# Kernel optimization log

Hardware: AMD Instinct MI355X
Metric: run time of the kernel (lower is better)

The kernel has to match this reference:

```python
import jax, jax.numpy as jnp
import numpy as np

N_RAYS, N_SAMPLES, N_VERTS = 2048, 32, 6890

def setup_inputs() -> dict:
    key = jax.random.key(0)
    k1, k2, k3, k4 = jax.random.split(key, 4)
    rays_points_world = jax.random.normal(k1, (1, N_RAYS, 1, N_SAMPLES, 3), jnp.float32)
    rays_directions_world = jax.random.normal(k2, (1, N_RAYS, 1, N_SAMPLES, 3), jnp.float32)
    vertices_posed = jax.random.normal(k3, (1, N_VERTS, 3), jnp.float32)
    # Ts must be invertible: small perturbation of identity (like rigid bone transforms)
    Ts = jax.random.normal(k4, (1, N_VERTS, 4, 4), jnp.float32) * 0.1 + jnp.eye(4, dtype=jnp.float32)
    return {
        'rays_points_world': rays_points_world,
        'rays_directions_world': rays_directions_world,
        'vertices_posed': vertices_posed,
        'Ts': Ts,
    }

def reference(rays_points_world, rays_directions_world, vertices_posed, Ts):
    orig_shape = rays_points_world.shape  # [1, R, 1, S, 3]
    pts = rays_points_world.reshape(-1, 3)          # (N, 3), N = R*S
    verts = vertices_posed[0]                       # (V, 3)
    # squared Euclidean distances via expansion (avoids N x V x 3 intermediate)
    d2 = ((pts * pts).sum(-1, keepdims=True)
          - 2.0 * (pts @ verts.T)
          + (verts * verts).sum(-1)[None, :])       # (N, V)
    idx = jnp.argmin(d2, axis=-1)                   # (N,) nearest vertex per point
    T_inv = jnp.linalg.inv(Ts)[0]                   # (V, 4, 4)
    T_sel = T_inv[idx]                              # (N, 4, 4) gather
    # flip x,y signs, build homogeneous coords
    xyz = jnp.stack([-pts[:, 0], -pts[:, 1], pts[:, 2]], axis=-1)      # (N, 3)
    homo = jnp.concatenate([xyz, jnp.ones_like(xyz[:, :1])], axis=-1)  # (N, 4)
    can = jnp.einsum('nij,nj->ni', T_sel, homo)[:, :3]                 # (N, 3)
    can = can.reshape(orig_shape)                                      # [1, R, 1, S, 3]
    # direction = finite diff along sample axis, last repeated
    dirs = can[..., 1:, :] - can[..., :-1, :]
    dirs = jnp.concatenate([dirs, dirs[..., -1:, :]], axis=-2)
    norm = jnp.linalg.norm(dirs, axis=-1, keepdims=True)
    dirs = dirs / jnp.maximum(norm, 1e-12)  # matches torch F.normalize eps
    flip = jnp.array([-1.0, -1.0, 1.0], dtype=can.dtype)
    return can * flip, dirs * flip
```

## Files before the change

kernel.cpp:

```cpp
#include <hip/hip_runtime.h>
#include <math.h>
#include <stdint.h>

#define N_RAYS    2048
#define N_SAMPLES 32
#define NPTS      (N_RAYS * N_SAMPLES)
#define NV        6890
#define G         32
#define NCELLS    (G * G * G)
#define SPLIT     8
#define RMAX      3
#define QMASK     0xFFFFE000u
#define IMASK     0x1FFFu
#define CMASK     0x1FFFu

#define TIE_REL   3e-3f
#define TIE_ABS   2e-5f

#define WS_COUNT     0
#define WS_FBC       4
#define WS_PARAMS    16
#define WS_HIST      128
#define WS_ROWMASK   (WS_HIST + 4 * NCELLS)
#define WS_CELLINFO  (WS_ROWMASK + 4 * G * G)
#define WS_SVERTS    (WS_CELLINFO + 4 * NCELLS)
#define WS_ORIGIDX   (WS_SVERTS + 16 * NV)
#define WS_LIST      (WS_ORIGIDX + 2 * NV + 12)
#define WS_NEEDED    (WS_LIST + 2 * NPTS)
#define WS_IDX       WS_HIST
#define WS_ZERO_W    ((WS_CELLINFO) / 4)

__device__ __forceinline__ uint64_t umin64(uint64_t a, uint64_t b) { return a < b ? a : b; }
__device__ __forceinline__ uint64_t umax64(uint64_t a, uint64_t b) { return a < b ? b : a; }

__device__ __forceinline__ int cell_clamp(float x, float org, float ih) {
    int c = (int)floorf((x - org) * ih);
    return min(max(c, 0), G - 1);
}

__global__ __launch_bounds__(256) void init_kernel(const float* __restrict__ verts,
                                                   float* __restrict__ params,
                                                   uint32_t* __restrict__ wzero) {
    const int t = threadIdx.x;
    if (blockIdx.x != 0) {
        for (int i = (blockIdx.x - 1) * 256 + t; i < WS_ZERO_W; i += (gridDim.x - 1) * 256) {
            if (i >= 4 && i < 32) continue;
            wzero[i] = 0u;
        }
        return;
    }
    __shared__ float mn[3][256], mx[3][256];
    float lmn[3] = {1e30f, 1e30f, 1e30f}, lmx[3] = {-1e30f, -1e30f, -1e30f};
    for (int v = t; v < NV; v += 256) {
        #pragma unroll
        for (int d = 0; d < 3; ++d) {
            float x = verts[v * 3 + d];
            lmn[d] = fminf(lmn[d], x); lmx[d] = fmaxf(lmx[d], x);
        }
    }
    #pragma unroll
    for (int d = 0; d < 3; ++d) { mn[d][t] = lmn[d]; mx[d][t] = lmx[d]; }
    __syncthreads();
    for (int s = 128; s > 0; s >>= 1) {
        if (t < s) {
            #pragma unroll
            for (int d = 0; d < 3; ++d) {
                mn[d][t] = fminf(mn[d][t], mn[d][t + s]);
                mx[d][t] = fmaxf(mx[d][t], mx[d][t + s]);
            }
        }
        __syncthreads();
    }
    if (t == 0) {
        #pragma unroll
        for (int d = 0; d < 3; ++d) {
            const float lo = mn[d][0] - 1e-3f, hi = mx[d][0] + 1e-3f;
            const float span = fmaxf(hi - lo, 1e-2f);
            params[d]     = lo;
            params[3 + d] = span / (float)G;
            params[6 + d] = (float)G / span;
        }
    }
}

__global__ void hist_kernel(const float* __restrict__ verts, const float* __restrict__ params,
                            uint32_t* __restrict__ hist) {
    const int v = blockIdx.x * blockDim.x + threadIdx.x;
    if (v >= NV) return;
    const int cx = cell_clamp(verts[v * 3 + 0], params[0], params[6]);
    const int cy = cell_clamp(verts[v * 3 + 1], params[1], params[7]);
    const int cz = cell_clamp(verts[v * 3 + 2], params[2], params[8]);
    atomicAdd(&hist[(cz * G + cy) * G + cx], 1u);
}

__global__ __launch_bounds__(1024) void scan_cells_kernel(const uint32_t* __restrict__ hist,
                                                          uint32_t* __restrict__ cellinfo,
                                                          uint32_t* __restrict__ rowmask) {
    __shared__ uint32_t wsum[16];
    const int t = threadIdx.x;
    const int lane = t & 63, wv = t >> 6;
    uint32_t loc[32];
    uint32_t sum = 0, rmask = 0;
    const int base = t * 32;
    #pragma unroll
    for (int i = 0; i < 32; ++i) {
        const uint32_t h = hist[base + i];
        loc[i] = sum; sum += h;
        if (h) rmask |= (1u << i);
    }
    rowmask[t] = rmask;
    uint32_t inc = sum;
    #pragma unroll
    for (int off = 1; off < 64; off <<= 1) {
        const uint32_t v = __shfl_up(inc, off);
        if (lane >= off) inc += v;
    }
    if (lane == 63) wsum[wv] = inc;
    __syncthreads();
    if (t < 16) {
        const uint32_t v = wsum[t];
        uint32_t p = v;
        #pragma unroll
        for (int off = 1; off < 16; off <<= 1) {
            const uint32_t u = __shfl_up(p, off);
            if (t >= off) p += u;
        }
        wsum[t] = p - v;
    }
    __syncthreads();
    const uint32_t pre = wsum[wv] + (inc - sum);
    #pragma unroll
    for (int i = 0; i < 32; ++i) {
        const uint32_t nxt = (i == 31) ? sum : loc[i + 1];
        const uint32_t cnt = nxt - loc[i];
        cellinfo[base + i] = ((pre + loc[i]) << 13) | cnt;
    }
}

__global__ void scatter_kernel(const float* __restrict__ verts, const float* __restrict__ params,
                               uint32_t* __restrict__ hist, const uint32_t* __restrict__ cellinfo,
                               float4* __restrict__ sverts, uint16_t* __restrict__ origidx) {
    const int v = blockIdx.x * blockDim.x + threadIdx.x;
    if (v >= NV) return;
    const float x = verts[v * 3 + 0], y = verts[v * 3 + 1], z = verts[v * 3 + 2];
    const int cx = cell_clamp(x, params[0], params[6]);
    const int cy = cell_clamp(y, params[1], params[7]);
    const int cz = cell_clamp(z, params[2], params[8]);
    const int c = (cz * G + cy) * G + cx;
    const uint32_t old = atomicSub(&hist[c], 1u);
    const uint32_t pos = (cellinfo[c] >> 13) + old - 1u;
    sverts[pos] = make_float4(x, y, z, fmaf(x, x, fmaf(y, y, z * z)));
    origidx[pos] = (uint16_t)v;
}

__global__ __launch_bounds__(256) void search_kernel(
    const float* __restrict__ pts, const float* __restrict__ params,
    const uint32_t* __restrict__ rowmask, const uint32_t* __restrict__ cellinfo,
    const float4* __restrict__ sverts, const uint16_t* __restrict__ origidx,
    uint16_t* __restrict__ idx16, uint16_t* __restrict__ list16,
    uint32_t* __restrict__ count, uint32_t* __restrict__ fbcount)
{
    __shared__ uint32_t srow[G * G];
    const int tid = threadIdx.x;
    for (int i = tid; i < G * G; i += 256) srow[i] = rowmask[i];
    __syncthreads();

    const int gtid = blockIdx.x * 256 + tid;
    const int sub  = gtid & (SPLIT - 1);
    const int n    = gtid / SPLIT;
    const float px = pts[n * 3 + 0], py = pts[n * 3 + 1], pz = pts[n * 3 + 2];
    const float acc = -0.5f * fmaf(px, px, fmaf(py, py, pz * pz));
    const float org0 = params[0], org1 = params[1], org2 = params[2];
    const float h0 = params[3], h1 = params[4], h2 = params[5];
    const int cx = cell_clamp(px, org0, params[6]);
    const int cy = cell_clamp(py, org1, params[7]);
    const int cz = cell_clamp(pz, org2, params[8]);

    uint32_t k1 = ~0u, k2 = ~0u;
    bool unproven = true;

    auto scan_run = [&](int rowG, int a, int b) {
        const uint32_t i0 = cellinfo[rowG + a];
        const uint32_t i1 = cellinfo[rowG + b];
        const uint32_t s = i0 >> 13;
        const uint32_t e = (i1 >> 13) + (i1 & CMASK);
        for (uint32_t j = s + sub; j < e; j += SPLIT) {
            const float4 q = sverts[j];
            const float dot = fmaf(px, q.x, fmaf(py, q.y, fmaf(pz, q.z, acc)));
            const float d = fmaxf(fmaf(-2.f, dot, q.w), 0.f);
            const uint32_t k = (__float_as_uint(d) & QMASK) | j;
            k2 = min(k2, max(k1, k)); k1 = min(k1, k);
        }
    };
    auto proven = [&](int xl, int xh, int yl, int yh, int zl, int zh) -> bool {
        uint32_t m1 = k1;
        #pragma unroll
        for (int off = 1; off < SPLIT; off <<= 1)
            m1 = min(m1, (uint32_t)__shfl_xor((int)m1, off));
        if (m1 == ~0u) return false;
        float dmin = 1e30f;
        bool any = false;
        if (xl > 0)     { dmin = fminf(dmin, px - fmaf((float)xl,      h0, org0)); any = true; }
        if (xh < G - 1) { dmin = fminf(dmin, fmaf((float)(xh + 1), h0, org0) - px); any = true; }
        if (yl > 0)     { dmin = fminf(dmin, py - fmaf((float)yl,      h1, org1)); any = true; }
        if (yh < G - 1) { dmin = fminf(dmin, fmaf((float)(yh + 1), h1, org1) - py); any = true; }
        if (zl > 0)     { dmin = fminf(dmin, pz - fmaf((float)zl,      h2, org2)); any = true; }
        if (zh < G - 1) { dmin = fminf(dmin, fmaf((float)(zh + 1), h2, org2) - pz); any = true; }
        if (!any) return true;
        const float dout = fmaxf(dmin, 0.f);
        const float d1f = __uint_as_float(m1 & QMASK);
        return dout * dout > fmaf(d1f, 1.05f, 1e-3f);
    };

    const int xlo1 = max(cx - 1, 0), xhi1 = min(cx + 1, G - 1);
    const int ylo1 = max(cy - 1, 0), yhi1 = min(cy + 1, G - 1);
    const int zlo1 = max(cz - 1, 0), zhi1 = min(cz + 1, G - 1);
    {
        const uint32_t wm = (uint32_t)((((uint64_t)1 << (xhi1 - xlo1 + 1)) - 1) << xlo1);
        for (int z = zlo1; z <= zhi1; ++z)
            for (int y = ylo1; y <= yhi1; ++y) {
                const int row = z * G + y;
                if (srow[row] & wm) scan_run(row * G, xlo1, xhi1);
            }
    }
    if (proven(xlo1, xhi1, ylo1, yhi1, zlo1, zhi1)) unproven = false;

    if (unproven) {
        for (int r = 2; r <= RMAX; ++r) {
            const int xlo = max(cx - r, 0), xhi = min(cx + r, G - 1);
            const int ylo = max(cy - r, 0), yhi = min(cy + r, G - 1);
            const int zlo = max(cz - r, 0), zhi = min(cz + r, G - 1);
            const uint32_t wm = (uint32_t)((((uint64_t)1 << (xhi - xlo + 1)) - 1) << xlo);
            for (int z = zlo; z <= zhi; ++z) {
                const int az = abs(z - cz);
                for (int y = ylo; y <= yhi; ++y) {
                    const int row = z * G + y;
                    const int ayz = max(abs(y - cy), az);
                    if (ayz == r) {
                        if (srow[row] & wm) scan_run(row * G, xlo, xhi);
                    } else {
                        #pragma unroll
                        for (int side = 0; side < 2; ++side) {
                            const int x = side ? cx + r : cx - r;
                            if (x < 0 || x > G - 1) continue;
                            if (!((srow[row] >> x) & 1u)) continue;
                            scan_run(row * G, x, x);
                        }
                    }
                }
            }
            if (proven(xlo, xhi, ylo, yhi, zlo, zhi)) { unproven = false; break; }
        }
    }

    #pragma unroll
    for (int off = 1; off < SPLIT; off <<= 1) {
        const uint32_t o1 = (uint32_t)__shfl_xor((int)k1, off);
        const uint32_t o2 = (uint32_t)__shfl_xor((int)k2, off);
        k2 = min(min(k2, o2), max(k1, o1)); k1 = min(k1, o1);
    }

    if (sub == 0) {
        if (unproven) {
            const uint32_t p = atomicAdd(fbcount, 1u);
            list16[NPTS - 1 - p] = (uint16_t)n;
        } else {
            const float d1 = __uint_as_float(k1 & QMASK);
            const float d2 = __uint_as_float(k2 & QMASK);
            idx16[n] = origidx[k1 & IMASK];
            if (d2 - d1 < fmaf(TIE_REL, d1, TIE_ABS)) {
                const uint32_t p = atomicAdd(count, 1u);
                list16[p] = (uint16_t)n;
            }
        }
    }
}

__global__ __launch_bounds__(256) void fixup_kernel(
    const float* __restrict__ pts,
    const float4* __restrict__ sverts, const uint16_t* __restrict__ origidx,
    uint16_t* __restrict__ list16,
    const uint32_t* __restrict__ count, const uint32_t* __restrict__ fbcount,
    uint16_t* __restrict__ idx16)
{
    const uint32_t fcnt = *fbcount;
    const uint32_t tcnt = *count;
    const uint32_t total = fcnt + tcnt;
    const int wv = threadIdx.x >> 6, lane = threadIdx.x & 63;
    for (uint32_t jj = blockIdx.x * 4 + wv; jj < total; jj += gridDim.x * 4) {
        const bool isFb = jj < fcnt;
        const int n = isFb ? (int)list16[NPTS - 1 - jj] : (int)list16[jj - fcnt];
        const float px = pts[n * 3 + 0], py = pts[n * 3 + 1], pz = pts[n * 3 + 2];
        bool needF64 = true;
        if (isFb) {
            const float acc = -0.5f * fmaf(px, px, fmaf(py, py, pz * pz));
            uint32_t k1 = ~0u, k2 = ~0u;
            int v = lane;
            for (; v + 192 < NV; v += 256) {
                const float4 q0 = sverts[v];
                const float4 q1 = sverts[v + 64];
                const float4 q2 = sverts[v + 128];
                const float4 q3 = sverts[v + 192];
                float dot, d; uint32_t k;
                dot = fmaf(px, q0.x, fmaf(py, q0.y, fmaf(pz, q0.z, acc)));
                d = fmaxf(fmaf(-2.f, dot, q0.w), 0.f);
                k = (__float_as_uint(d) & QMASK) | (uint32_t)v;
                k2 = min(k2, max(k1, k)); k1 = min(k1, k);
                dot = fmaf(px, q1.x, fmaf(py, q1.y, fmaf(pz, q1.z, acc)));
                d = fmaxf(fmaf(-2.f, dot, q1.w), 0.f);
                k = (__float_as_uint(d) & QMASK) | (uint32_t)(v + 64);
                k2 = min(k2, max(k1, k)); k1 = min(k1, k);
                dot = fmaf(px, q2.x, fmaf(py, q2.y, fmaf(pz, q2.z, acc)));
                d = fmaxf(fmaf(-2.f, dot, q2.w), 0.f);
                k = (__float_as_uint(d) & QMASK) | (uint32_t)(v + 128);
                k2 = min(k2, max(k1, k)); k1 = min(k1, k);
                dot = fmaf(px, q3.x, fmaf(py, q3.y, fmaf(pz, q3.z, acc)));
                d = fmaxf(fmaf(-2.f, dot, q3.w), 0.f);
                k = (__float_as_uint(d) & QMASK) | (uint32_t)(v + 192);
                k2 = min(k2, max(k1, k)); k1 = min(k1, k);
            }
            for (; v < NV; v += 64) {
                const float4 q = sverts[v];
                const float dot = fmaf(px, q.x, fmaf(py, q.y, fmaf(pz, q.z, acc)));
                const float d = fmaxf(fmaf(-2.f, dot, q.w), 0.f);
                const uint32_t k = (__float_as_uint(d) & QMASK) | (uint32_t)v;
                k2 = min(k2, max(k1, k)); k1 = min(k1, k);
            }
            #pragma unroll
            for (int off = 1; off < 64; off <<= 1) {
                const uint32_t o1 = (uint32_t)__shfl_xor((int)k1, off);
                const uint32_t o2 = (uint32_t)__shfl_xor((int)k2, off);
                k2 = min(min(k2, o2), max(k1, o1)); k1 = min(k1, o1);
            }
            const float d1 = __uint_as_float(k1 & QMASK);
            const float d2 = __uint_as_float(k2 & QMASK);
            needF64 = (d2 - d1 < fmaf(TIE_REL, d1, TIE_ABS));
            if (!needF64 && lane == 0) idx16[n] = origidx[k1 & IMASK];
        }
        if (needF64) {
            const double pxd = (double)px, pyd = (double)py, pzd = (double)pz;
            double best = 1e300; uint32_t bi = 0xFFFFFFFFu;
            int v = lane;
            for (; v + 192 < NV; v += 256) {
                const float4 q0 = sverts[v];
                const float4 q1 = sverts[v + 64];
                const float4 q2 = sverts[v + 128];
                const float4 q3 = sverts[v + 192];
                const uint32_t o0 = origidx[v];
                const uint32_t o1 = origidx[v + 64];
                const uint32_t o2 = origidx[v + 128];
                const uint32_t o3 = origidx[v + 192];
                double dx, dy, dz, d;
                dx = pxd - (double)q0.x; dy = pyd - (double)q0.y; dz = pzd - (double)q0.z;
                d = dx*dx + dy*dy + dz*dz;
                if (d < best || (d == best && o0 < bi)) { best = d; bi = o0; }
                dx = pxd - (double)q1.x; dy = pyd - (double)q1.y; dz = pzd - (double)q1.z;
                d = dx*dx + dy*dy + dz*dz;
                if (d < best || (d == best && o1 < bi)) { best = d; bi = o1; }
                dx = pxd - (double)q2.x; dy = pyd - (double)q2.y; dz = pzd - (double)q2.z;
                d = dx*dx + dy*dy + dz*dz;
                if (d < best || (d == best && o2 < bi)) { best = d; bi = o2; }
                dx = pxd - (double)q3.x; dy = pyd - (double)q3.y; dz = pzd - (double)q3.z;
                d = dx*dx + dy*dy + dz*dz;
                if (d < best || (d == best && o3 < bi)) { best = d; bi = o3; }
            }
            for (; v < NV; v += 64) {
                const float4 q = sverts[v];
                const uint32_t oi = origidx[v];
                const double dx = pxd - (double)q.x;
                const double dy = pyd - (double)q.y;
                const double dz = pzd - (double)q.z;
                const double d = dx*dx + dy*dy + dz*dz;
                if (d < best || (d == best && oi < bi)) { best = d; bi = oi; }
            }
            #pragma unroll
            for (int off = 1; off < 64; off <<= 1) {
                const double od = __shfl_xor(best, off);
                const uint32_t oi = (uint32_t)__shfl_xor((int)bi, off);
                if (od < best || (od == best && oi < bi)) { best = od; bi = oi; }
            }
            if (lane == 0) idx16[n] = (uint16_t)bi;
        }
    }
}

__global__ __launch_bounds__(256) void output_kernel(
    const float* __restrict__ pts, const float* __restrict__ Ts,
    const uint16_t* __restrict__ idx16, float* __restrict__ out)
{
    __shared__ double sc[256][3];
    const int tid = threadIdx.x;
    const int n = blockIdx.x * 256 + tid;
    const float px = pts[n*3+0], py = pts[n*3+1], pz = pts[n*3+2];
    const int v = (int)idx16[n];

    const float4* T4 = reinterpret_cast<const float4*>(Ts + (size_t)v * 16);
    const float4 r0 = T4[0], r1 = T4[1], r2 = T4[2], r3 = T4[3];
    const double m[16] = { r0.x, r0.y, r0.z, r0.w,  r1.x, r1.y, r1.z, r1.w,
                           r2.x, r2.y, r2.z, r2.w,  r3.x, r3.y, r3.z, r3.w };
    double inv[16];
    inv[0]  =  m[5]*m[10]*m[15] - m[5]*m[11]*m[14] - m[9]*m[6]*m[15] + m[9]*m[7]*m[14] + m[13]*m[6]*m[11] - m[13]*m[7]*m[10];
    inv[4]  = -m[4]*m[10]*m[15] + m[4]*m[11]*m[14] + m[8]*m[6]*m[15] - m[8]*m[7]*m[14] - m[12]*m[6]*m[11] + m[12]*m[7]*m[10];
    inv[8]  =  m[4]*m[9]*m[15] - m[4]*m[11]*m[13] - m[8]*m[5]*m[15] + m[8]*m[7]*m[13] + m[12]*m[5]*m[11] - m[12]*m[7]*m[9];
    inv[12] = -m[4]*m[9]*m[14] + m[4]*m[10]*m[13] + m[8]*m[5]*m[14] - m[8]*m[6]*m[13] - m[12]*m[5]*m[10] + m[12]*m[6]*m[9];
    inv[1]  = -m[1]*m[10]*m[15] + m[1]*m[11]*m[14] + m[9]*m[2]*m[15] - m[9]*m[3]*m[14] - m[13]*m[2]*m[11] + m[13]*m[3]*m[10];
    inv[5]  =  m[0]*m[10]*m[15] - m[0]*m[11]*m[14] - m[8]*m[2]*m[15] + m[8]*m[3]*m[14] + m[12]*m[2]*m[11] - m[12]*m[3]*m[10];
    inv[9]  = -m[0]*m[9]*m[15] + m[0]*m[11]*m[13] + m[8]*m[1]*m[15] - m[8]*m[3]*m[13] - m[12]*m[1]*m[11] + m[12]*m[3]*m[9];
    inv[13] =  m[0]*m[9]*m[14] - m[0]*m[10]*m[13] - m[8]*m[1]*m[14] + m[8]*m[2]*m[13] + m[12]*m[1]*m[10] - m[12]*m[2]*m[9];
    inv[2]  =  m[1]*m[6]*m[15] - m[1]*m[7]*m[14] - m[5]*m[2]*m[15] + m[5]*m[3]*m[14] + m[13]*m[2]*m[7] - m[13]*m[3]*m[6];
    inv[6]  = -m[0]*m[6]*m[15] + m[0]*m[7]*m[14] + m[4]*m[2]*m[15] - m[4]*m[3]*m[14] - m[12]*m[2]*m[7] + m[12]*m[3]*m[6];
    inv[10] =  m[0]*m[5]*m[15] - m[0]*m[7]*m[13] - m[4]*m[1]*m[15] + m[4]*m[3]*m[13] + m[12]*m[1]*m[7] - m[12]*m[3]*m[5];
    inv[14] = -m[0]*m[5]*m[14] + m[0]*m[6]*m[13] + m[4]*m[1]*m[14] - m[4]*m[2]*m[13] - m[12]*m[1]*m[6] + m[12]*m[2]*m[5];
    inv[3]  = -m[1]*m[6]*m[11] + m[1]*m[7]*m[10] + m[5]*m[2]*m[11] - m[5]*m[3]*m[10] - m[9]*m[2]*m[7] + m[9]*m[3]*m[6];
    inv[7]  =  m[0]*m[6]*m[11] - m[0]*m[7]*m[10] - m[4]*m[2]*m[11] + m[4]*m[3]*m[10] + m[8]*m[2]*m[7] - m[8]*m[3]*m[6];
    inv[11] = -m[0]*m[5]*m[11] + m[0]*m[7]*m[9] + m[4]*m[1]*m[11] - m[4]*m[3]*m[9] - m[8]*m[1]*m[7] + m[8]*m[3]*m[5];
    inv[15] =  m[0]*m[5]*m[10] - m[0]*m[6]*m[9] - m[4]*m[1]*m[10] + m[4]*m[2]*m[9] + m[8]*m[1]*m[6] - m[8]*m[2]*m[5];
    const double det = m[0]*inv[0] + m[1]*inv[4] + m[2]*inv[8] + m[3]*inv[12];
    const double rd = 1.0 / det;

    const double hx = -(double)px, hy = -(double)py, hz = (double)pz;
    const double c0 = (inv[0]*hx + inv[1]*hy + inv[2]*hz  + inv[3])  * rd;
    const double c1 = (inv[4]*hx + inv[5]*hy + inv[6]*hz  + inv[7])  * rd;
    const double c2 = (inv[8]*hx + inv[9]*hy + inv[10]*hz + inv[11]) * rd;
    const double f0 = -c0, f1 = -c1, f2 = c2;

    out[n*3+0] = (float)f0; out[n*3+1] = (float)f1; out[n*3+2] = (float)f2;
    sc[tid][0] = f0; sc[tid][1] = f1; sc[tid][2] = f2;
    __syncthreads();

    int l0 = tid, l1 = tid + 1;
    if ((tid & (N_SAMPLES - 1)) == N_SAMPLES - 1) { l0 = tid - 1; l1 = tid; }
    const double dx = sc[l1][0] - sc[l0][0];
    const double dy = sc[l1][1] - sc[l0][1];
    const double dz = sc[l1][2] - sc[l0][2];
    const double nr = fmax(sqrt(dx*dx + dy*dy + dz*dz), 1e-12);
    float* o = out + (size_t)NPTS * 3 + (size_t)n * 3;
    o[0] = (float)(dx / nr); o[1] = (float)(dy / nr); o[2] = (float)(dz / nr);
}

__global__ void zero_kernel(uint32_t* __restrict__ w, int nwords) {
    for (int i = blockIdx.x * blockDim.x + threadIdx.x; i < nwords; i += gridDim.x * blockDim.x)
        w[i] = 0u;
}

__global__ __launch_bounds__(256) void scan_kernel(
    const float* __restrict__ pts, const float* __restrict__ verts,
    uint16_t* __restrict__ idx16, uint16_t* __restrict__ list16,
    uint32_t* __restrict__ count)
{
    __shared__ float4 sv[2048];
    const int tid  = threadIdx.x;
    const int part = tid & 7;
    const int grp  = tid >> 3;
    const int n0   = blockIdx.x * 64 + grp * 2;
    const float ax = pts[n0*3+0], ay = pts[n0*3+1], az = pts[n0*3+2];
    const float bx = pts[n0*3+3], by = pts[n0*3+4], bz = pts[n0*3+5];
    const float acc = -0.5f * fmaf(ax, ax, fmaf(ay, ay, az*az));
    const float bcc = -0.5f * fmaf(bx, bx, fmaf(by, by, bz*bz));
    uint64_t ak1 = ~0ull, ak2 = ~0ull, bk1 = ~0ull, bk2 = ~0ull;
    for (int base = 0; base < NV; base += 2048) {
        const int cnt = min(NV - base, 2048);
        __syncthreads();
        for (int v = tid; v < cnt; v += 256) {
            const float x = verts[(base+v)*3+0], y = verts[(base+v)*3+1], z = verts[(base+v)*3+2];
            sv[v] = make_float4(x, y, z, fmaf(x, x, fmaf(y, y, z*z)));
        }
        __syncthreads();
        #pragma unroll 4
        for (int v = part; v < cnt; v += 8) {
            const float4 q = sv[v];
            const uint64_t vi = (uint64_t)(base + v);
            float s, d; uint64_t k;
            s = fmaf(ax, q.x, fmaf(ay, q.y, fmaf(az, q.z, acc)));
            d = fmaxf(fmaf(-2.f, s, q.w), 0.f);
            k = ((uint64_t)__float_as_uint(d) << 32) | vi;
            ak2 = umin64(ak2, umax64(ak1, k)); ak1 = umin64(ak1, k);
            s = fmaf(bx, q.x, fmaf(by, q.y, fmaf(bz, q.z, bcc)));
            d = fmaxf(fmaf(-2.f, s, q.w), 0.f);
            k = ((uint64_t)__float_as_uint(d) << 32) | vi;
            bk2 = umin64(bk2, umax64(bk1, k)); bk1 = umin64(bk1, k);
        }
    }
    #pragma unroll
    for (int off = 1; off < 8; off <<= 1) {
        uint64_t o1, o2;
        o1 = __shfl_xor((unsigned long long)ak1, off); o2 = __shfl_xor((unsigned long long)ak2, off);
        ak2 = umin64(umin64(ak2, o2), umax64(ak1, o1)); ak1 = umin64(ak1, o1);
        o1 = __shfl_xor((unsigned long long)bk1, off); o2 = __shfl_xor((unsigned long long)bk2, off);
        bk2 = umin64(umin64(bk2, o2), umax64(bk1, o1)); bk1 = umin64(bk1, o1);
    }
    if (part == 0) {
        const float ad1 = __uint_as_float((uint32_t)(ak1 >> 32));
        const float ad2 = __uint_as_float((uint32_t)(ak2 >> 32));
        idx16[n0] = (uint16_t)(ak1 & 0xFFFFu);
        if (ad2 - ad1 < fmaf(1e-4f, ad1, TIE_ABS)) { uint32_t p = atomicAdd(count, 1u); list16[p] = (uint16_t)n0; }
        const float bd1 = __uint_as_float((uint32_t)(bk1 >> 32));
        const float bd2 = __uint_as_float((uint32_t)(bk2 >> 32));
        idx16[n0+1] = (uint16_t)(bk1 & 0xFFFFu);
        if (bd2 - bd1 < fmaf(1e-4f, bd1, TIE_ABS)) { uint32_t p = atomicAdd(count, 1u); list16[p] = (uint16_t)(n0+1); }
    }
}

__global__ __launch_bounds__(256) void refine_kernel(
    const float* __restrict__ pts, const float* __restrict__ verts,
    const uint16_t* __restrict__ list16, const uint32_t* __restrict__ count,
    uint16_t* __restrict__ idx16)
{
    const uint32_t cnt = *count;
    const int wv = threadIdx.x >> 6, lane = threadIdx.x & 63;
    for (uint32_t j = blockIdx.x * 4 + wv; j < cnt; j += gridDim.x * 4) {
        const int n = (int)list16[j];
        const double px = (double)pts[n*3+0];
        const double py = (double)pts[n*3+1];
        const double pz = (double)pts[n*3+2];
        double best = 1e300; uint32_t bi = 0xFFFFFFFFu;
        for (int v = lane; v < NV; v += 64) {
            const double dx = px - (double)verts[v*3+0];
            const double dy = py - (double)verts[v*3+1];
            const double dz = pz - (double)verts[v*3+2];
            const double d = dx*dx + dy*dy + dz*dz;
            if (d < best || (d == best && (uint32_t)v < bi)) { best = d; bi = (uint32_t)v; }
        }
        #pragma unroll
        for (int off = 1; off < 64; off <<= 1) {
            const double od = __shfl_xor(best, off);
            const uint32_t oi = (uint32_t)__shfl_xor((int)bi, off);
            if (od < best || (od == best && oi < bi)) { best = od; bi = oi; }
        }
        if (lane == 0) idx16[n] = (uint16_t)bi;
    }
}

extern "C" void kernel_launch(void* const* d_in, const int* in_sizes, int n_in,
                              void* d_out, int out_size, void* d_ws, size_t ws_size,
                              hipStream_t stream) {
    const float* pts   = (const float*)d_in[0];
    const float* verts = (const float*)d_in[2];
    const float* Ts    = (const float*)d_in[3];
    float* out = (float*)d_out;

    uint8_t* ws = (uint8_t*)d_ws;
    uint32_t* count   = (uint32_t*)(ws + WS_COUNT);
    uint32_t* fbcount = (uint32_t*)(ws + WS_FBC);

    if (ws_size >= (size_t)WS_NEEDED) {
        float*    params   = (float*)(ws + WS_PARAMS);
        uint32_t* hist     = (uint32_t*)(ws + WS_HIST);
        uint32_t* rowmask  = (uint32_t*)(ws + WS_ROWMASK);
        uint32_t* cellinfo = (uint32_t*)(ws + WS_CELLINFO);
        float4*   sverts   = (float4*)(ws + WS_SVERTS);
        uint16_t* origidx  = (uint16_t*)(ws + WS_ORIGIDX);
        uint16_t* idx16    = (uint16_t*)(ws + WS_IDX);
        uint16_t* list16   = (uint16_t*)(ws + WS_LIST);
        const int vblocks = (NV + 255) / 256;

        hipLaunchKernelGGL(init_kernel, dim3(65), dim3(256), 0, stream,
                           verts, params, (uint32_t*)ws);
        hipLaunchKernelGGL(hist_kernel, dim3(vblocks), dim3(256), 0, stream,
                           verts, params, hist);
        hipLaunchKernelGGL(scan_cells_kernel, dim3(1), dim3(1024), 0, stream,
                           hist, cellinfo, rowmask);
        hipLaunchKernelGGL(scatter_kernel, dim3(vblocks), dim3(256), 0, stream,
                           verts, params, hist, cellinfo, sverts, origidx);
        hipLaunchKernelGGL(search_kernel, dim3(NPTS * SPLIT / 256), dim3(256), 0, stream,
                           pts, params, rowmask, cellinfo, sverts, origidx,
                           idx16, list16, count, fbcount);
        hipLaunchKernelGGL(fixup_kernel, dim3(1024), dim3(256), 0, stream,
                           pts, sverts, origidx, list16, count, fbcount, idx16);
        hipLaunchKernelGGL(output_kernel, dim3(NPTS / 256), dim3(256), 0, stream,
                           pts, Ts, idx16, out);
    } else {
        uint16_t* idx16  = (uint16_t*)(ws + 64);
        uint16_t* list16 = (uint16_t*)(ws + 64 + 2 * NPTS);
        hipLaunchKernelGGL(zero_kernel, dim3(1), dim3(64), 0, stream, (uint32_t*)ws, 1);
        hipLaunchKernelGGL(scan_kernel, dim3(NPTS / 64), dim3(256), 0, stream,
                           pts, verts, idx16, list16, count);
        hipLaunchKernelGGL(refine_kernel, dim3(512), dim3(256), 0, stream,
                           pts, verts, list16, count, idx16);
        hipLaunchKernelGGL(output_kernel, dim3(NPTS / 256), dim3(256), 0, stream,
                           pts, Ts, idx16, out);
    }
}
```

Before: 82.22 us.

## Sort query points by grid cell before nearest-vertex search

Adds a counting sort of query points by voxel cell, built alongside the vertex histogram, prefix scan and scatter, and lets the search kernel process points in that cell order. Neighbouring threads then scan the same cells, which should cut wavefront divergence and improve cache reuse of the sorted vertices. In exchange the point histogram and scatter add atomics over all 65k points, and the setup kernels now launch NPTS/256 blocks. It only takes effect if the workspace is large enough for the extra buffers.

New measurement: 104.0 us. 1.26x slower.

```diff
diff --git a/kernel.cpp b/kernel.cpp
--- a/kernel.cpp
+++ b/kernel.cpp
@@ -27,6 +27,9 @@
 #define WS_ORIGIDX   (WS_SVERTS + 16 * NV)
 #define WS_LIST      (WS_ORIGIDX + 2 * NV + 12)
 #define WS_NEEDED    (WS_LIST + 2 * NPTS)
+#define WS_PHIST     (WS_NEEDED)
+#define WS_ORDER     (WS_PHIST + 4 * NCELLS)
+#define WS_NEEDED2   (WS_ORDER + 2 * NPTS)
 #define WS_IDX       WS_HIST
 #define WS_ZERO_W    ((WS_CELLINFO) / 4)
 
@@ -40,12 +43,17 @@
 
 __global__ __launch_bounds__(256) void init_kernel(const float* __restrict__ verts,
                                                    float* __restrict__ params,
-                                                   uint32_t* __restrict__ wzero) {
+                                                   uint32_t* __restrict__ wzero,
+                                                   uint32_t* __restrict__ phist) {
     const int t = threadIdx.x;
     if (blockIdx.x != 0) {
         for (int i = (blockIdx.x - 1) * 256 + t; i < WS_ZERO_W; i += (gridDim.x - 1) * 256) {
             if (i >= 4 && i < 32) continue;
             wzero[i] = 0u;
+        }
+        if (phist) {
+            for (int i = (blockIdx.x - 1) * 256 + t; i < NCELLS; i += (gridDim.x - 1) * 256)
+                phist[i] = 0u;
         }
         return;
     }
@@ -83,6 +91,28 @@
     }
 }
 
+__global__ __launch_bounds__(256) void hist2_kernel(
+    const float* __restrict__ verts, const float* __restrict__ pts,
+    const float* __restrict__ params,
+    uint32_t* __restrict__ hist, uint32_t* __restrict__ phist)
+{
+    const int i = blockIdx.x * blockDim.x + threadIdx.x;
+    const float og0 = params[0], og1 = params[1], og2 = params[2];
+    const float ih0 = params[6], ih1 = params[7], ih2 = params[8];
+    if (i < NV) {
+        const int cx = cell_clamp(verts[i * 3 + 0], og0, ih0);
+        const int cy = cell_clamp(verts[i * 3 + 1], og1, ih1);
+        const int cz = cell_clamp(verts[i * 3 + 2], og2, ih2);
+        atomicAdd(&hist[(cz * G + cy) * G + cx], 1u);
+    }
+    if (i < NPTS) {
+        const int cx = cell_clamp(pts[i * 3 + 0], og0, ih0);
+        const int cy = cell_clamp(pts[i * 3 + 1], og1, ih1);
+        const int cz = cell_clamp(pts[i * 3 + 2], og2, ih2);
+        if (phist) atomicAdd(&phist[(cz * G + cy) * G + cx], 1u);
+    }
+}
+
 __global__ void hist_kernel(const float* __restrict__ verts, const float* __restrict__ params,
                             uint32_t* __restrict__ hist) {
     const int v = blockIdx.x * blockDim.x + threadIdx.x;
@@ -91,6 +121,66 @@
     const int cy = cell_clamp(verts[v * 3 + 1], params[1], params[7]);
     const int cz = cell_clamp(verts[v * 3 + 2], params[2], params[8]);
     atomicAdd(&hist[(cz * G + cy) * G + cx], 1u);
+}
+
+__global__ __launch_bounds__(1024) void scan2_kernel(const uint32_t* __restrict__ hist,
+                                                     uint32_t* __restrict__ cellinfo,
+                                                     uint32_t* __restrict__ rowmask,
+                                                     uint32_t* __restrict__ phist) {
+    __shared__ uint32_t wsum[16], wsum2[16];
+    const int t = threadIdx.x;
+    const int lane = t & 63, wv = t >> 6;
+    uint32_t loc[32];
+    uint32_t sum = 0, rmask = 0, sum2 = 0;
+    const int base = t * 32;
+    #pragma unroll
+    for (int i = 0; i < 32; ++i) {
+        const uint32_t h = hist[base + i];
+        loc[i] = sum; sum += h;
+        if (h) rmask |= (1u << i);
+    }
+    rowmask[t] = rmask;
+    if (phist) {
+        #pragma unroll
+        for (int i = 0; i < 32; ++i) sum2 += phist[base + i];
+    }
+    uint32_t inc = sum, inc2 = sum2;
+    #pragma unroll
+    for (int off = 1; off < 64; off <<= 1) {
+        const uint32_t v = __shfl_up(inc, off);
+        const uint32_t v2 = __shfl_up(inc2, off);
+        if (lane >= off) { inc += v; inc2 += v2; }
+    }
+    if (lane == 63) { wsum[wv] = inc; wsum2[wv] = inc2; }
+    __syncthreads();
+    if (t < 16) {
+        const uint32_t v = wsum[t], v2 = wsum2[t];
+        uint32_t p = v, p2 = v2;
+        #pragma unroll
+        for (int off = 1; off < 16; off <<= 1) {
+            const uint32_t u = __shfl_up(p, off);
+            const uint32_t u2 = __shfl_up(p2, off);
+            if (t >= off) { p += u; p2 += u2; }
+        }
+        wsum[t] = p - v; wsum2[t] = p2 - v2;
+    }
+    __syncthreads();
+    const uint32_t pre = wsum[wv] + (inc - sum);
+    #pragma unroll
+    for (int i = 0; i < 32; ++i) {
+        const uint32_t nxt = (i == 31) ? sum : loc[i + 1];
+        const uint32_t cnt = nxt - loc[i];
+        cellinfo[base + i] = ((pre + loc[i]) << 13) | cnt;
+    }
+    if (phist) {
+        uint32_t run = wsum2[wv] + (inc2 - sum2);
+        #pragma unroll
+        for (int i = 0; i < 32; ++i) {
+            const uint32_t c = phist[base + i];
+            phist[base + i] = run;
+            run += c;
+        }
+    }
 }
 
 __global__ __launch_bounds__(1024) void scan_cells_kernel(const uint32_t* __restrict__ hist,
@@ -134,6 +224,37 @@
         const uint32_t nxt = (i == 31) ? sum : loc[i + 1];
         const uint32_t cnt = nxt - loc[i];
         cellinfo[base + i] = ((pre + loc[i]) << 13) | cnt;
+    }
+}
+
+__global__ __launch_bounds__(256) void scatter2_kernel(
+    const float* __restrict__ verts, const float* __restrict__ pts,
+    const float* __restrict__ params,
+    uint32_t* __restrict__ hist, const uint32_t* __restrict__ cellinfo,
+    float4* __restrict__ sverts, uint16_t* __restrict__ origidx,
+    uint32_t* __restrict__ phist, uint16_t* __restrict__ order16)
+{
+    const int i = blockIdx.x * blockDim.x + threadIdx.x;
+    const float og0 = params[0], og1 = params[1], og2 = params[2];
+    const float ih0 = params[6], ih1 = params[7], ih2 = params[8];
+    if (i < NV) {
+        const float x = verts[i * 3 + 0], y = verts[i * 3 + 1], z = verts[i * 3 + 2];
+        const int cx = cell_clamp(x, og0, ih0);
+        const int cy = cell_clamp(y, og1, ih1);
+        const int cz = cell_clamp(z, og2, ih2);
+        const int c = (cz * G + cy) * G + cx;
+        const uint32_t old = atomicSub(&hist[c], 1u);
+        const uint32_t pos = (cellinfo[c] >> 13) + old - 1u;
+        sverts[pos] = make_float4(x, y, z, fmaf(x, x, fmaf(y, y, z * z)));
+        origidx[pos] = (uint16_t)i;
+    }
+    if (i < NPTS && phist) {
+        const int cx = cell_clamp(pts[i * 3 + 0], og0, ih0);
+        const int cy = cell_clamp(pts[i * 3 + 1], og1, ih1);
+        const int cz = cell_clamp(pts[i * 3 + 2], og2, ih2);
+        const int c = (cz * G + cy) * G + cx;
+        const uint32_t pos = atomicAdd(&phist[c], 1u);
+        order16[pos] = (uint16_t)i;
     }
 }
 
@@ -157,6 +278,7 @@
     const float* __restrict__ pts, const float* __restrict__ params,
     const uint32_t* __restrict__ rowmask, const uint32_t* __restrict__ cellinfo,
     const float4* __restrict__ sverts, const uint16_t* __restrict__ origidx,
+    const uint16_t* __restrict__ order16,
     uint16_t* __restrict__ idx16, uint16_t* __restrict__ list16,
     uint32_t* __restrict__ count, uint32_t* __restrict__ fbcount)
 {
@@ -167,7 +289,8 @@
 
     const int gtid = blockIdx.x * 256 + tid;
     const int sub  = gtid & (SPLIT - 1);
-    const int n    = gtid / SPLIT;
+    const int q    = gtid / SPLIT;
+    const int n    = order16 ? (int)order16[q] : q;
     const float px = pts[n * 3 + 0], py = pts[n * 3 + 1], pz = pts[n * 3 + 2];
     const float acc = -0.5f * fmaf(px, px, fmaf(py, py, pz * pz));
     const float org0 = params[0], org1 = params[1], org2 = params[2];
@@ -185,9 +308,9 @@
         const uint32_t s = i0 >> 13;
         const uint32_t e = (i1 >> 13) + (i1 & CMASK);
         for (uint32_t j = s + sub; j < e; j += SPLIT) {
-            const float4 q = sverts[j];
-            const float dot = fmaf(px, q.x, fmaf(py, q.y, fmaf(pz, q.z, acc)));
-            const float d = fmaxf(fmaf(-2.f, dot, q.w), 0.f);
+            const float4 qv = sverts[j];
+            const float dot = fmaf(px, qv.x, fmaf(py, qv.y, fmaf(pz, qv.z, acc)));
+            const float d = fmaxf(fmaf(-2.f, dot, qv.w), 0.f);
             const uint32_t k = (__float_as_uint(d) & QMASK) | j;
             k2 = min(k2, max(k1, k)); k1 = min(k1, k);
         }
@@ -552,18 +675,31 @@
         uint16_t* origidx  = (uint16_t*)(ws + WS_ORIGIDX);
         uint16_t* idx16    = (uint16_t*)(ws + WS_IDX);
         uint16_t* list16   = (uint16_t*)(ws + WS_LIST);
+        const bool sorted  = ws_size >= (size_t)WS_NEEDED2;
+        uint32_t* phist    = sorted ? (uint32_t*)(ws + WS_PHIST) : nullptr;
+        uint16_t* order16  = sorted ? (uint16_t*)(ws + WS_ORDER) : nullptr;
         const int vblocks = (NV + 255) / 256;
 
         hipLaunchKernelGGL(init_kernel, dim3(65), dim3(256), 0, stream,
-                           verts, params, (uint32_t*)ws);
-        hipLaunchKernelGGL(hist_kernel, dim3(vblocks), dim3(256), 0, stream,
-                           verts, params, hist);
-        hipLaunchKernelGGL(scan_cells_kernel, dim3(1), dim3(1024), 0, stream,
-                           hist, cellinfo, rowmask);
-        hipLaunchKernelGGL(scatter_kernel, dim3(vblocks), dim3(256), 0, stream,
-                           verts, params, hist, cellinfo, sverts, origidx);
+                           verts, params, (uint32_t*)ws, phist);
+        if (sorted) {
+            hipLaunchKernelGGL(hist2_kernel, dim3(NPTS / 256), dim3(256), 0, stream,
+                               verts, pts, params, hist, phist);
+            hipLaunchKernelGGL(scan2_kernel, dim3(1), dim3(1024), 0, stream,
+                               hist, cellinfo, rowmask, phist);
+            hipLaunchKernelGGL(scatter2_kernel, dim3(NPTS / 256), dim3(256), 0, stream,
+                               verts, pts, params, hist, cellinfo, sverts, origidx,
+                               phist, order16);
+        } else {
+            hipLaunchKernelGGL(hist_kernel, dim3(vblocks), dim3(256), 0, stream,
+                               verts, params, hist);
+            hipLaunchKernelGGL(scan_cells_kernel, dim3(1), dim3(1024), 0, stream,
+                               hist, cellinfo, rowmask);
+            hipLaunchKernelGGL(scatter_kernel, dim3(vblocks), dim3(256), 0, stream,
+                               verts, params, hist, cellinfo, sverts, origidx);
+        }
         hipLaunchKernelGGL(search_kernel, dim3(NPTS * SPLIT / 256), dim3(256), 0, stream,
-                           pts, params, rowmask, cellinfo, sverts, origidx,
+                           pts, params, rowmask, cellinfo, sverts, origidx, order16,
                            idx16, list16, count, fbcount);
         hipLaunchKernelGGL(fixup_kernel, dim3(1024), dim3(256), 0, stream,
                            pts, sverts, origidx, list16, count, fbcount, idx16);
```
